# Performance work log

Measured on AMD Instinct MI355X. Metric: run time of the kernel, lower is better.

Reference implementation:

```python
import jax, jax.numpy as jnp
import numpy as np

BIT = 8
QMAX = 2 ** (BIT - 1) - 1          # 127
QMIN = -(2 ** (BIT - 1))           # -128
BOUNDARY_RANGE = 0.005
EPS = 1e-5


def _quant_act_int8(x):
    # StatsQ per-tensor activation quantization: scale from (1 - boundary_range)
    # quantile of |x| (robust absmax), fake-quant with STE.
    amax = jnp.maximum(jnp.quantile(jnp.abs(x), 1.0 - BOUNDARY_RANGE), EPS)
    s = QMAX / amax
    q = jnp.clip(jnp.round(x * s), QMIN, QMAX) / s
    return x + jax.lax.stop_gradient(q - x)


def _quant_w_ternary(w):
    # BitNet-1.58-style per-tensor ternary weight quantization:
    # gamma = mean(|W|); W_q in {-1, 0, +1} * gamma; STE.
    gamma = jnp.mean(jnp.abs(w)) + EPS
    q = jnp.clip(jnp.round(w / gamma), -1.0, 1.0) * gamma
    return w + jax.lax.stop_gradient(q - w)


def _qlinear(x, w):
    # quantize activations (int8 fake-quant) and weights (ternary), then matmul
    xq = _quant_act_int8(x)
    wq = _quant_w_ternary(w)
    return jnp.einsum('btd,hd->bth', xq, wq)


def _layernorm(x, g, b):
    mu = jnp.mean(x, axis=-1, keepdims=True)
    var = jnp.mean(jnp.square(x - mu), axis=-1, keepdims=True)
    return (x - mu) * jax.lax.rsqrt(var + 1e-5) * g + b


def setup_inputs() -> dict:
    key = jax.random.key(0)
    k_x, k_w1, k_w2 = jax.random.split(key, 3)
    B, T, D, H = 64, 256, 1024, 4096
    x = jax.random.normal(k_x, (B, T, D), dtype=jnp.float32)
    ln_g = jnp.ones((D,), dtype=jnp.float32)
    ln_b = jnp.zeros((D,), dtype=jnp.float32)
    w1 = jax.random.normal(k_w1, (H, D), dtype=jnp.float32) * (1.0 / np.sqrt(D))
    w2 = jax.random.normal(k_w2, (D, H), dtype=jnp.float32) * (1.0 / np.sqrt(H))
    return {'x': x, 'ln_g': ln_g, 'ln_b': ln_b, 'w1': w1, 'w2': w2}


def reference(x, ln_g, ln_b, w1, w2):
    h = _layernorm(x, ln_g, ln_b)          # [B,T,D]
    h = _qlinear(h, w1)                    # [B,T,H]
    h = jax.nn.gelu(h, approximate=False)  # torch nn.GELU default = exact erf
    out = _qlinear(h, w2)                  # [B,T,D]
    return out
```

## Files before the change

### kernel.cpp

```cpp
#include <hip/hip_runtime.h>
#include <hip/hip_fp16.h>
#include <math.h>


#define M_ROWS 16384
#define D_DIM  1024
#define H_DIM  4096

typedef int i32x4 __attribute__((ext_vector_type(4)));
typedef int i32x16 __attribute__((ext_vector_type(16)));

#define AS1 __attribute__((address_space(1)))
#define AS3 __attribute__((address_space(3)))

__device__ __forceinline__ void load_lds16(const void* g, void* l) {
  __builtin_amdgcn_global_load_lds((const AS1 void*)g, (AS3 void*)l, 16, 0, 0);
}

__device__ __forceinline__ float block_sum256(float v, float* lds) {
#pragma unroll
  for (int o = 32; o > 0; o >>= 1) v += __shfl_down(v, o, 64);
  int t = threadIdx.x;
  __syncthreads();
  if ((t & 63) == 0) lds[t >> 6] = v;
  __syncthreads();
  return lds[0] + lds[1] + lds[2] + lds[3];
}

__global__ __launch_bounds__(256) void k_layernorm(
    const float* __restrict__ x, const float* __restrict__ g,
    const float* __restrict__ b, __half* __restrict__ out) {
  __shared__ float lds[4];
  int row = blockIdx.x, t = threadIdx.x;
  float4 v = ((const float4*)(x + (size_t)row * D_DIM))[t];
  float s = v.x + v.y + v.z + v.w;
  s = block_sum256(s, lds);
  float mu = s * (1.0f / D_DIM);
  float d0 = v.x - mu, d1 = v.y - mu, d2 = v.z - mu, d3 = v.w - mu;
  float ss = d0 * d0 + d1 * d1 + d2 * d2 + d3 * d3;
  ss = block_sum256(ss, lds);
  float inv = 1.0f / sqrtf(ss * (1.0f / D_DIM) + 1e-5f);
  float4 gg = ((const float4*)g)[t];
  float4 bb = ((const float4*)b)[t];
  __half2 p0 = __floats2half2_rn(d0 * inv * gg.x + bb.x, d1 * inv * gg.y + bb.y);
  __half2 p1 = __floats2half2_rn(d2 * inv * gg.z + bb.z, d3 * inv * gg.w + bb.w);
  uint2 st;
  st.x = *(unsigned*)&p0;
  st.y = *(unsigned*)&p1;
  ((uint2*)(out + (size_t)row * D_DIM))[t] = st;
}

__global__ __launch_bounds__(256) void k_absmean2(const float4* __restrict__ w1,
                                                  const float4* __restrict__ w2,
                                                  size_t n4, double* __restrict__ out) {
  int which = (blockIdx.x >= (gridDim.x >> 1)) ? 1 : 0;
  const float4* p = which ? w2 : w1;
  unsigned half_grid = gridDim.x >> 1;
  unsigned blk = blockIdx.x - which * half_grid;
  double s = 0.0;
  size_t stride = (size_t)half_grid * blockDim.x;
  for (size_t i = (size_t)blk * blockDim.x + threadIdx.x; i < n4; i += stride) {
    float4 v = p[i];
    s += (double)fabsf(v.x) + (double)fabsf(v.y) + (double)fabsf(v.z) + (double)fabsf(v.w);
  }
#pragma unroll
  for (int o = 32; o > 0; o >>= 1) s += __shfl_down(s, o, 64);
  __shared__ double ds[4];
  int t = threadIdx.x;
  if ((t & 63) == 0) ds[t >> 6] = s;
  __syncthreads();
  if (t == 0) atomicAdd(out + which, ds[0] + ds[1] + ds[2] + ds[3]);
}

__device__ __forceinline__ int tern1(float w, float gamma) {
  return (int)fminf(1.f, fmaxf(-1.f, rintf(w / gamma)));
}

__global__ __launch_bounds__(256) void k_wquant2(const float4* __restrict__ w1,
                                                 const float4* __restrict__ w2,
                                                 unsigned* __restrict__ q1,
                                                 unsigned* __restrict__ q2, size_t n4,
                                                 const double* __restrict__ sump,
                                                 double inv_n, float* __restrict__ gamma_out) {
  int which = (blockIdx.x >= (gridDim.x >> 1)) ? 1 : 0;
  const float4* w = which ? w2 : w1;
  unsigned* wq = which ? q2 : q1;
  unsigned half_grid = gridDim.x >> 1;
  unsigned blk = blockIdx.x - which * half_grid;
  float gamma = (float)(sump[which] * inv_n) + 1e-5f;
  if (blk == 0 && threadIdx.x == 0) gamma_out[which] = gamma;
  size_t stride = (size_t)half_grid * blockDim.x;
  for (size_t i = (size_t)blk * blockDim.x + threadIdx.x; i < n4; i += stride) {
    float4 v = w[i];
    int a = tern1(v.x, gamma), b = tern1(v.y, gamma), c = tern1(v.z, gamma), d = tern1(v.w, gamma);
    wq[i] = (unsigned)(a & 255) | ((unsigned)(b & 255) << 8) |
            ((unsigned)(c & 255) << 16) | ((unsigned)(d & 255) << 24);
  }
}

__global__ __launch_bounds__(512) void k_hist16(const uint4* __restrict__ p, size_t n8,
                                                unsigned* __restrict__ hist) {
  extern __shared__ unsigned h[];
  int t = threadIdx.x;
  for (int i = t; i < 32768; i += 512) h[i] = 0;
  __syncthreads();
  size_t stride = (size_t)gridDim.x * 512;
  for (size_t i = (size_t)blockIdx.x * 512 + t; i < n8; i += stride) {
    uint4 u = p[i];
    atomicAdd(&h[u.x & 0x7FFFu], 1u);
    atomicAdd(&h[(u.x >> 16) & 0x7FFFu], 1u);
    atomicAdd(&h[u.y & 0x7FFFu], 1u);
    atomicAdd(&h[(u.y >> 16) & 0x7FFFu], 1u);
    atomicAdd(&h[u.z & 0x7FFFu], 1u);
    atomicAdd(&h[(u.z >> 16) & 0x7FFFu], 1u);
    atomicAdd(&h[u.w & 0x7FFFu], 1u);
    atomicAdd(&h[(u.w >> 16) & 0x7FFFu], 1u);
  }
  __syncthreads();
  for (int i = t; i < 32768; i += 512) {
    unsigned c = h[i];
    if (c) atomicAdd(&hist[i], c);
  }
}

__global__ __launch_bounds__(256) void k_scanq(const unsigned* __restrict__ hist,
                                               float* __restrict__ scl,
                                               unsigned long long k, double frac) {
  __shared__ unsigned tsum[256];
  __shared__ unsigned long long pre[256];
  __shared__ unsigned vk, vk1;
  int t = threadIdx.x;
  unsigned s = 0;
  for (int j = 0; j < 128; ++j) s += hist[t * 128 + j];
  tsum[t] = s;
  __syncthreads();
  if (t == 0) {
    unsigned long long c = 0;
    for (int i = 0; i < 256; ++i) { pre[i] = c; c += tsum[i]; }
  }
  __syncthreads();
  unsigned long long base = pre[t];
  for (int j = 0; j < 128; ++j) {
    unsigned c = hist[t * 128 + j];
    if (base <= k && k < base + c) vk = t * 128 + j;
    if (base <= k + 1 && k + 1 < base + c) vk1 = t * 128 + j;
    base += c;
  }
  __syncthreads();
  if (t == 0) {
    double a = (double)__half2float(__ushort_as_half((unsigned short)vk));
    double b = (double)__half2float(__ushort_as_half((unsigned short)vk1));
    double qv = (frac >= 0.5) ? (b - (b - a) * (1.0 - frac)) : (a + (b - a) * frac);
    float amax = fmaxf((float)qv, 1e-5f);
    scl[0] = amax;
    scl[1] = 127.0f / amax;
  }
}

__device__ __forceinline__ void unpack8(uint4 u, float* f) {
  __half2 h;
  h = *(__half2*)&u.x; f[0] = __low2float(h); f[1] = __high2float(h);
  h = *(__half2*)&u.y; f[2] = __low2float(h); f[3] = __high2float(h);
  h = *(__half2*)&u.z; f[4] = __low2float(h); f[5] = __high2float(h);
  h = *(__half2*)&u.w; f[6] = __low2float(h); f[7] = __high2float(h);
}

__device__ __forceinline__ unsigned qpack4(float a, float b, float c, float d, float s) {
  int qa = (int)fminf(127.f, fmaxf(-128.f, rintf(a * s)));
  int qb = (int)fminf(127.f, fmaxf(-128.f, rintf(b * s)));
  int qc = (int)fminf(127.f, fmaxf(-128.f, rintf(c * s)));
  int qd = (int)fminf(127.f, fmaxf(-128.f, rintf(d * s)));
  return (unsigned)(qa & 255) | ((unsigned)(qb & 255) << 8) |
         ((unsigned)(qc & 255) << 16) | ((unsigned)(qd & 255) << 24);
}

__global__ __launch_bounds__(256) void k_quant16(const uint4* __restrict__ p,
                                                 uint2* __restrict__ q, size_t n8,
                                                 const float* __restrict__ scl) {
  float s = scl[1];
  size_t stride = (size_t)gridDim.x * blockDim.x;
  for (size_t i = (size_t)blockIdx.x * blockDim.x + threadIdx.x; i < n8; i += stride) {
    float f[8];
    unpack8(p[i], f);
    uint2 r;
    r.x = qpack4(f[0], f[1], f[2], f[3], s);
    r.y = qpack4(f[4], f[5], f[6], f[7], s);
    q[i] = r;
  }
}

__device__ __forceinline__ float gelu_fast(float v) {
  float a = fabsf(v) * 0.70710678118654752f;
  float t = __builtin_amdgcn_rcpf(fmaf(0.3275911f, a, 1.0f));
  float p = t * fmaf(t, fmaf(t, fmaf(t, fmaf(t, 1.061405429f, -1.453152027f),
                                     1.421413741f), -0.284496736f), 0.254829592f);
  float e = __expf(-a * a);
  float er = fmaf(-p, e, 1.0f);
  float erf_s = copysignf(er, v);
  return 0.5f * v * (1.0f + erf_s);
}

template <int K, bool GELU>
__global__ __launch_bounds__(256, 4) void k_gemm(const signed char* __restrict__ A,
                                                 const signed char* __restrict__ B,
                                                 int N, void* __restrict__ outp,
                                                 const float* __restrict__ gamma_p,
                                                 const float* __restrict__ scl) {
  __shared__ __align__(16) signed char As[16384];
  __shared__ __align__(16) signed char Bs[16384];
  const int t = threadIdx.x;
  const int l = t & 63;
  const int wv = t >> 6;
  const int wr = (wv >> 1) * 64, wc = (wv & 1) * 64;
  const int m0 = blockIdx.y * 128, n0 = blockIdx.x * 128;

  const signed char* ag[4]; const signed char* bg[4];
  signed char* al[4]; signed char* bl[4];
#pragma unroll
  for (int c = 0; c < 4; ++c) {
    int g = c * 256 + t;
    int r = g >> 3;
    int cg = (g & 7) ^ (r & 7);
    ag[c] = A + (size_t)(m0 + r) * K + cg * 16;
    bg[c] = B + (size_t)(n0 + r) * K + cg * 16;
    al[c] = As + g * 16;
    bl[c] = Bs + g * 16;
  }

  int a_off[2][4], b_off[2][4];
#pragma unroll
  for (int mi = 0; mi < 2; ++mi)
#pragma unroll
    for (int ks = 0; ks < 4; ++ks) {
      int am = wr + mi * 32 + (l & 31);
      int g = 2 * ks + (l >> 5);
      a_off[mi][ks] = am * 128 + (g ^ (am & 7)) * 16;
      int bn = wc + mi * 32 + (l & 31);
      b_off[mi][ks] = bn * 128 + (g ^ (bn & 7)) * 16;
    }

  i32x16 acc[2][2];
#pragma unroll
  for (int mi = 0; mi < 2; ++mi)
#pragma unroll
    for (int ni = 0; ni < 2; ++ni)
      acc[mi][ni] = (i32x16)(0);

  for (int kk = 0; kk < K; kk += 512) {
#pragma unroll
    for (int j = 0; j < 4; ++j) {
      const int ko = j * 128;
      __syncthreads();
#pragma unroll
      for (int c = 0; c < 4; ++c) {
        load_lds16(ag[c] + kk + ko, al[c]);
        load_lds16(bg[c] + kk + ko, bl[c]);
      }
      __syncthreads();
#pragma unroll
      for (int ks = 0; ks < 4; ++ks) {
        i32x4 af[2], bf[2];
#pragma unroll
        for (int i = 0; i < 2; ++i) af[i] = *(const i32x4*)(As + a_off[i][ks]);
#pragma unroll
        for (int i = 0; i < 2; ++i) bf[i] = *(const i32x4*)(Bs + b_off[i][ks]);
#pragma unroll
        for (int mi = 0; mi < 2; ++mi)
#pragma unroll
          for (int ni = 0; ni < 2; ++ni)
            acc[mi][ni] = __builtin_amdgcn_mfma_i32_32x32x32_i8(af[mi], bf[ni], acc[mi][ni], 0, 0, 0);
      }
    }
  }

  const float cs = (*gamma_p) / scl[1];
  const int col0 = n0 + wc + (l & 31);
  const int row0 = m0 + wr + 4 * (l >> 5);
#pragma unroll
  for (int mi = 0; mi < 2; ++mi) {
#pragma unroll
    for (int ni = 0; ni < 2; ++ni) {
      int col = col0 + ni * 32;
#pragma unroll
      for (int reg = 0; reg < 16; ++reg) {
        int row = row0 + mi * 32 + (reg & 3) + 8 * (reg >> 2);
        float v = cs * (float)acc[mi][ni][reg];
        size_t idx = (size_t)row * N + col;
        if (GELU) {
          ((__half*)outp)[idx] = __float2half(gelu_fast(v));
        } else {
          ((float*)outp)[idx] = v;
        }
      }
    }
  }
}

extern "C" void kernel_launch(void* const* d_in, const int* in_sizes, int n_in,
                              void* d_out, int out_size, void* d_ws, size_t ws_size,
                              hipStream_t stream) {
  const float* x = (const float*)d_in[0];
  const float* ln_g = (const float*)d_in[1];
  const float* ln_b = (const float*)d_in[2];
  const float* w1 = (const float*)d_in[3];
  const float* w2 = (const float*)d_in[4];
  float* out = (float*)d_out;

  char* ws = (char*)d_ws;
  __half* h2 = (__half*)ws;
  __half* h1 = (__half*)(ws + ((size_t)128 << 20));
  signed char* xq1 = (signed char*)(ws + ((size_t)160 << 20));
  signed char* xq2 = (signed char*)(ws + ((size_t)128 << 20));
  signed char* w1q = (signed char*)(ws + ((size_t)192 << 20));
  signed char* w2q = (signed char*)(ws + ((size_t)196 << 20));
  char* sm = ws + ((size_t)200 << 20);
  unsigned* hista = (unsigned*)sm;
  unsigned* histb = (unsigned*)(sm + (128 << 10));
  double* wsum = (double*)(sm + (256 << 10));
  float* gamma = (float*)(sm + (256 << 10) + 16);
  float* scl1 = (float*)(sm + (256 << 10) + 32);
  float* scl2 = (float*)(sm + (256 << 10) + 40);

  hipMemsetAsync(sm, 0, (256 << 10) + 64, stream);
  hipFuncSetAttribute((const void*)k_hist16, hipFuncAttributeMaxDynamicSharedMemorySize,
                      131072);

  const double qq = 1.0 - 0.005;
  const unsigned long long N1 = (unsigned long long)M_ROWS * D_DIM;
  const unsigned long long N2 = (unsigned long long)M_ROWS * H_DIM;
  double idx1 = qq * (double)(N1 - 1);
  double idx2 = qq * (double)(N2 - 1);
  unsigned long long k1 = (unsigned long long)idx1;
  unsigned long long k2 = (unsigned long long)idx2;
  double frac1 = idx1 - (double)k1;
  double frac2 = idx2 - (double)k2;

  const size_t nW4 = (size_t)H_DIM * D_DIM / 4;
  const double inv_nW = 1.0 / (double)(H_DIM * D_DIM);

  k_absmean2<<<1024, 256, 0, stream>>>((const float4*)w1, (const float4*)w2, nW4, wsum);
  k_wquant2<<<2048, 256, 0, stream>>>((const float4*)w1, (const float4*)w2,
                                      (unsigned*)w1q, (unsigned*)w2q, nW4, wsum, inv_nW, gamma);

  k_layernorm<<<M_ROWS, 256, 0, stream>>>(x, ln_g, ln_b, h1);

  const size_t n8_1 = N1 / 8;
  k_hist16<<<256, 512, 131072, stream>>>((const uint4*)h1, n8_1, hista);
  k_scanq<<<1, 256, 0, stream>>>(hista, scl1, k1, frac1);
  k_quant16<<<1024, 256, 0, stream>>>((const uint4*)h1, (uint2*)xq1, n8_1, scl1);

  k_gemm<D_DIM, true><<<dim3(H_DIM / 128, M_ROWS / 128), 256, 0, stream>>>(
      xq1, w1q, H_DIM, (void*)h2, gamma + 0, scl1);

  const size_t n8_2 = N2 / 8;
  k_hist16<<<256, 512, 131072, stream>>>((const uint4*)h2, n8_2, histb);
  k_scanq<<<1, 256, 0, stream>>>(histb, scl2, k2, frac2);
  k_quant16<<<2048, 256, 0, stream>>>((const uint4*)h2, (uint2*)xq2, n8_2, scl2);

  k_gemm<H_DIM, false><<<dim3(D_DIM / 128, M_ROWS / 128), 256, 0, stream>>>(
      xq2, w2q, D_DIM, (void*)out, gamma + 1, scl2);
}
```

Measured before the change: 482.0 us.

## Restructure int8 GEMM into 256x256 tiles with 4-stage async LDS pipeline

Rewrites the int8 MFMA GEMM to use 512-thread blocks computing 256x256 output tiles, with a 4-deep ring of LDS buffers (128KB dynamic shared) filled by direct global-to-LDS loads issued three K-steps ahead. It also applies an XCD-aware block index swizzle and raises wave priority around MFMA bursts. The goal is to hide global load latency, cut barrier stalls and improve data reuse per block. The cost is lower occupancy (large LDS use, 2 waves per SIMD at most) and a more fragile hand-tuned vmcnt and barrier schedule.

Measured after the change: 494.7 us. 2.6% more time.

```diff
diff --git a/kernel.cpp b/kernel.cpp
--- a/kernel.cpp
+++ b/kernel.cpp
@@ -201,89 +201,135 @@
 }
 
 template <int K, bool GELU>
-__global__ __launch_bounds__(256, 4) void k_gemm(const signed char* __restrict__ A,
+__global__ __launch_bounds__(512, 2) void k_gemm(const signed char* __restrict__ A,
                                                  const signed char* __restrict__ B,
                                                  int N, void* __restrict__ outp,
                                                  const float* __restrict__ gamma_p,
                                                  const float* __restrict__ scl) {
-  __shared__ __align__(16) signed char As[16384];
-  __shared__ __align__(16) signed char Bs[16384];
-  const int t = threadIdx.x;
-  const int l = t & 63;
-  const int wv = t >> 6;
-  const int wr = (wv >> 1) * 64, wc = (wv & 1) * 64;
-  const int m0 = blockIdx.y * 128, n0 = blockIdx.x * 128;
-
-  const signed char* ag[4]; const signed char* bg[4];
-  signed char* al[4]; signed char* bl[4];
-#pragma unroll
-  for (int c = 0; c < 4; ++c) {
-    int g = c * 256 + t;
-    int r = g >> 3;
-    int cg = (g & 7) ^ (r & 7);
-    ag[c] = A + (size_t)(m0 + r) * K + cg * 16;
-    bg[c] = B + (size_t)(n0 + r) * K + cg * 16;
-    al[c] = As + g * 16;
-    bl[c] = Bs + g * 16;
-  }
-
-  int a_off[2][4], b_off[2][4];
-#pragma unroll
-  for (int mi = 0; mi < 2; ++mi)
-#pragma unroll
-    for (int ks = 0; ks < 4; ++ks) {
-      int am = wr + mi * 32 + (l & 31);
-      int g = 2 * ks + (l >> 5);
-      a_off[mi][ks] = am * 128 + (g ^ (am & 7)) * 16;
-      int bn = wc + mi * 32 + (l & 31);
-      b_off[mi][ks] = bn * 128 + (g ^ (bn & 7)) * 16;
+  constexpr int NT = K / 64;
+  extern __shared__ __align__(16) char smem[];
+  signed char* As = (signed char*)smem;
+  signed char* Bs = (signed char*)smem + 65536;
+
+  const int tid = threadIdx.x;
+  const int lane = tid & 63;
+  const int wv = tid >> 6;
+  const int wr = (wv >> 2) * 128;
+  const int wc = (wv & 3) * 64;
+
+  const unsigned nwg = gridDim.x;
+  const unsigned q8 = nwg >> 3;
+  const unsigned bid = blockIdx.x;
+  const unsigned swz = (bid & 7) * q8 + (bid >> 3);
+  const unsigned nx = (unsigned)N >> 8;
+  const int n0 = (int)(swz % nx) * 256;
+  const int m0 = (int)(swz / nx) * 256;
+
+  const int srow0 = tid >> 2;
+  const int srow1 = srow0 + 128;
+  const int scg = (tid & 3) ^ ((srow0 >> 1) & 3);
+  const signed char* aG0 = A + (size_t)(m0 + srow0) * K + scg * 16;
+  const signed char* aG1 = A + (size_t)(m0 + srow1) * K + scg * 16;
+  const signed char* bG0 = B + (size_t)(n0 + srow0) * K + scg * 16;
+  const signed char* bG1 = B + (size_t)(n0 + srow1) * K + scg * 16;
+  const int sL0 = tid * 16;
+  const int sL1 = sL0 + 8192;
+
+#define STAGE_A(t_) { const int bo_ = ((t_) & 3) * 16384;            \
+    load_lds16(aG0 + (size_t)(t_) * 64, As + bo_ + sL0);             \
+    load_lds16(aG1 + (size_t)(t_) * 64, As + bo_ + sL1); }
+#define STAGE_B(t_) { const int bo_ = ((t_) & 3) * 16384;            \
+    load_lds16(bG0 + (size_t)(t_) * 64, Bs + bo_ + sL0);             \
+    load_lds16(bG1 + (size_t)(t_) * 64, Bs + bo_ + sL1); }
+
+  int a_off[4][2], b_off[2][2];
+#pragma unroll
+  for (int mi = 0; mi < 4; ++mi) {
+    int am = wr + mi * 32 + (lane & 31);
+#pragma unroll
+    for (int ksl = 0; ksl < 2; ++ksl) {
+      int g = ksl * 2 + (lane >> 5);
+      a_off[mi][ksl] = am * 64 + ((g ^ ((am >> 1) & 3)) << 4);
     }
-
-  i32x16 acc[2][2];
-#pragma unroll
-  for (int mi = 0; mi < 2; ++mi)
-#pragma unroll
-    for (int ni = 0; ni < 2; ++ni)
-      acc[mi][ni] = (i32x16)(0);
-
-  for (int kk = 0; kk < K; kk += 512) {
-#pragma unroll
-    for (int j = 0; j < 4; ++j) {
-      const int ko = j * 128;
-      __syncthreads();
-#pragma unroll
-      for (int c = 0; c < 4; ++c) {
-        load_lds16(ag[c] + kk + ko, al[c]);
-        load_lds16(bg[c] + kk + ko, bl[c]);
-      }
-      __syncthreads();
-#pragma unroll
-      for (int ks = 0; ks < 4; ++ks) {
-        i32x4 af[2], bf[2];
-#pragma unroll
-        for (int i = 0; i < 2; ++i) af[i] = *(const i32x4*)(As + a_off[i][ks]);
-#pragma unroll
-        for (int i = 0; i < 2; ++i) bf[i] = *(const i32x4*)(Bs + b_off[i][ks]);
-#pragma unroll
-        for (int mi = 0; mi < 2; ++mi)
-#pragma unroll
-          for (int ni = 0; ni < 2; ++ni)
-            acc[mi][ni] = __builtin_amdgcn_mfma_i32_32x32x32_i8(af[mi], bf[ni], acc[mi][ni], 0, 0, 0);
-      }
+  }
+#pragma unroll
+  for (int ni = 0; ni < 2; ++ni) {
+    int bn = wc + ni * 32 + (lane & 31);
+#pragma unroll
+    for (int ksl = 0; ksl < 2; ++ksl) {
+      int g = ksl * 2 + (lane >> 5);
+      b_off[ni][ksl] = bn * 64 + ((g ^ ((bn >> 1) & 3)) << 4);
     }
   }
 
+  i32x16 acc[4][2];
+#pragma unroll
+  for (int mi = 0; mi < 4; ++mi)
+#pragma unroll
+    for (int ni = 0; ni < 2; ++ni) acc[mi][ni] = (i32x16)(0);
+
+  STAGE_A(0); STAGE_B(0);
+  STAGE_A(1); STAGE_B(1);
+  STAGE_A(2); STAGE_B(2);
+  asm volatile("s_waitcnt vmcnt(8)" ::: "memory");
+  __builtin_amdgcn_s_barrier();
+
+#pragma unroll 4
+  for (int t = 0; t < NT; ++t) {
+    const int bo = (t & 3) * 16384;
+    {
+      i32x4 af[4], bf[2];
+#pragma unroll
+      for (int mi = 0; mi < 4; ++mi) af[mi] = *(const i32x4*)(As + bo + a_off[mi][0]);
+#pragma unroll
+      for (int ni = 0; ni < 2; ++ni) bf[ni] = *(const i32x4*)(Bs + bo + b_off[ni][0]);
+      if (t + 3 < NT) STAGE_A(t + 3);
+      __builtin_amdgcn_sched_barrier(0);
+      __builtin_amdgcn_s_barrier();
+      __builtin_amdgcn_s_setprio(1);
+#pragma unroll
+      for (int mi = 0; mi < 4; ++mi)
+#pragma unroll
+        for (int ni = 0; ni < 2; ++ni)
+          acc[mi][ni] = __builtin_amdgcn_mfma_i32_32x32x32_i8(af[mi], bf[ni], acc[mi][ni], 0, 0, 0);
+      __builtin_amdgcn_s_setprio(0);
+    }
+    {
+      i32x4 af[4], bf[2];
+#pragma unroll
+      for (int mi = 0; mi < 4; ++mi) af[mi] = *(const i32x4*)(As + bo + a_off[mi][1]);
+#pragma unroll
+      for (int ni = 0; ni < 2; ++ni) bf[ni] = *(const i32x4*)(Bs + bo + b_off[ni][1]);
+      if (t + 3 < NT) STAGE_B(t + 3);
+      __builtin_amdgcn_sched_barrier(0);
+      __builtin_amdgcn_s_barrier();
+      __builtin_amdgcn_s_setprio(1);
+#pragma unroll
+      for (int mi = 0; mi < 4; ++mi)
+#pragma unroll
+        for (int ni = 0; ni < 2; ++ni)
+          acc[mi][ni] = __builtin_amdgcn_mfma_i32_32x32x32_i8(af[mi], bf[ni], acc[mi][ni], 0, 0, 0);
+      __builtin_amdgcn_s_setprio(0);
+    }
+    if (t < NT - 3)       { asm volatile("s_waitcnt vmcnt(8)" ::: "memory"); }
+    else if (t == NT - 3) { asm volatile("s_waitcnt vmcnt(4)" ::: "memory"); }
+    else                  { asm volatile("s_waitcnt vmcnt(0)" ::: "memory"); }
+    __builtin_amdgcn_s_barrier();
+  }
+#undef STAGE_A
+#undef STAGE_B
+
   const float cs = (*gamma_p) / scl[1];
-  const int col0 = n0 + wc + (l & 31);
-  const int row0 = m0 + wr + 4 * (l >> 5);
-#pragma unroll
-  for (int mi = 0; mi < 2; ++mi) {
+  const int col0 = n0 + wc + (lane & 31);
+  const int row0 = m0 + wr + 4 * (lane >> 5);
+#pragma unroll
+  for (int mi = 0; mi < 4; ++mi) {
 #pragma unroll
     for (int ni = 0; ni < 2; ++ni) {
-      int col = col0 + ni * 32;
+      const int col = col0 + ni * 32;
 #pragma unroll
       for (int reg = 0; reg < 16; ++reg) {
-        int row = row0 + mi * 32 + (reg & 3) + 8 * (reg >> 2);
+        const int row = row0 + mi * 32 + (reg & 3) + 8 * (reg >> 2);
         float v = cs * (float)acc[mi][ni][reg];
         size_t idx = (size_t)row * N + col;
         if (GELU) {
@@ -324,6 +370,10 @@
   hipMemsetAsync(sm, 0, (256 << 10) + 64, stream);
   hipFuncSetAttribute((const void*)k_hist16, hipFuncAttributeMaxDynamicSharedMemorySize,
                       131072);
+  hipFuncSetAttribute((const void*)(k_gemm<D_DIM, true>),
+                      hipFuncAttributeMaxDynamicSharedMemorySize, 131072);
+  hipFuncSetAttribute((const void*)(k_gemm<H_DIM, false>),
+                      hipFuncAttributeMaxDynamicSharedMemorySize, 131072);
 
   const double qq = 1.0 - 0.005;
   const unsigned long long N1 = (unsigned long long)M_ROWS * D_DIM;
@@ -349,7 +399,7 @@
   k_scanq<<<1, 256, 0, stream>>>(hista, scl1, k1, frac1);
   k_quant16<<<1024, 256, 0, stream>>>((const uint4*)h1, (uint2*)xq1, n8_1, scl1);
 
-  k_gemm<D_DIM, true><<<dim3(H_DIM / 128, M_ROWS / 128), 256, 0, stream>>>(
+  k_gemm<D_DIM, true><<<(H_DIM / 256) * (M_ROWS / 256), 512, 131072, stream>>>(
       xq1, w1q, H_DIM, (void*)h2, gamma + 0, scl1);
 
   const size_t n8_2 = N2 / 8;
@@ -357,6 +407,6 @@
   k_scanq<<<1, 256, 0, stream>>>(histb, scl2, k2, frac2);
   k_quant16<<<2048, 256, 0, stream>>>((const uint4*)h2, (uint2*)xq2, n8_2, scl2);
 
-  k_gemm<H_DIM, false><<<dim3(D_DIM / 128, M_ROWS / 128), 256, 0, stream>>>(
+  k_gemm<H_DIM, false><<<(D_DIM / 256) * (M_ROWS / 256), 512, 131072, stream>>>(
       xq2, w2q, D_DIM, (void*)out, gamma + 1, scl2);
 }
```
